# Optimization experiments

Measured on AMD Instinct MI355X. Metric: run time of the kernel, lower is better.

The kernel has to match this reference:

```python
import jax, jax.numpy as jnp
import numpy as np

B = 131072
IN_FEATS = 32
STATE = 128


def setup_inputs() -> dict:
    key = jax.random.key(0)
    k1, k2, k3, k4, k5 = jax.random.split(key, 5)
    stdv = 1.0 / np.sqrt(STATE)
    return {
        "input": jax.random.normal(k1, (B, IN_FEATS), dtype=jnp.float32),
        "old_h": jax.random.normal(k2, (B, STATE), dtype=jnp.float32),
        "old_cell": jax.random.normal(k3, (B, STATE), dtype=jnp.float32),
        "weights": jax.random.uniform(k4, (3 * STATE, IN_FEATS + STATE), dtype=jnp.float32, minval=-stdv, maxval=stdv),
        "bias": jax.random.uniform(k5, (3 * STATE,), dtype=jnp.float32, minval=-stdv, maxval=stdv),
    }


def reference(input, old_h, old_cell, weights, bias):
    # X: [B, state+in_feats] (old_h first, matching torch.cat([old_h, input], 1))
    X = jnp.concatenate([old_h, input], axis=1)
    # gate_weights: [B, 3*state] = X @ W^T + b (F.linear semantics)
    gate_weights = jnp.einsum('bf,gf->bg', X, weights) + bias
    ig_pre, og_pre, cc_pre = jnp.split(gate_weights, 3, axis=1)
    input_gate = jax.nn.sigmoid(ig_pre)
    output_gate = jax.nn.sigmoid(og_pre)
    candidate_cell = jax.nn.elu(cc_pre)
    new_cell = old_cell + candidate_cell * input_gate
    new_h = jnp.tanh(new_cell) * output_gate
    return (new_h, new_cell)
```

## Files before the change

kernel.cpp:

```cpp
#include <hip/hip_runtime.h>

#define TOTAL_B   131072
#define IN_FEATS  32
#define STATE     128
#define KDIM      160
#define BROWS     64
#define THREADS   512
#define LDSROW    384
#define GRID      512
#define ITERS     ((TOTAL_B / BROWS) / GRID)

typedef __bf16 bf16x8 __attribute__((ext_vector_type(8)));
typedef float  f32x4  __attribute__((ext_vector_type(4)));

__device__ __forceinline__ float fsigmoid(float x) { return 1.0f / (1.0f + __expf(-x)); }
__device__ __forceinline__ float ftanh(float x)    { return 2.0f / (1.0f + __expf(-2.0f * x)) - 1.0f; }

struct Xregs {
    f32x4 hlo[2], hhi[2];
    f32x4 xlo, xhi;
};

__device__ __forceinline__ void issue_x(const float* __restrict__ old_h,
                                        const float* __restrict__ xin,
                                        long b0, int t, Xregs& r)
{
    #pragma unroll
    for (int i = 0; i < 2; ++i) {
        int c   = t + i * THREADS;
        int row = c >> 4;
        int kc  = (c & 15) * 8;
        const float* p = old_h + (b0 + row) * (long)STATE + kc;
        r.hlo[i] = *(const f32x4*)p;
        r.hhi[i] = *((const f32x4*)p + 1);
    }
    if (t < 256) {
        int row = t >> 2;
        int kc  = (t & 3) * 8;
        const float* p = xin + (b0 + row) * (long)IN_FEATS + kc;
        r.xlo = *(const f32x4*)p;
        r.xhi = *((const f32x4*)p + 1);
    }
}

__device__ __forceinline__ void write_x(char* smem, int t, const Xregs& r)
{
    #pragma unroll
    for (int i = 0; i < 2; ++i) {
        int c   = t + i * THREADS;
        int row = c >> 4;
        int kc  = (c & 15) * 8;
        bf16x8 v;
        #pragma unroll
        for (int j = 0; j < 4; ++j) { v[j] = (__bf16)r.hlo[i][j]; v[j + 4] = (__bf16)r.hhi[i][j]; }
        int off = row * LDSROW + kc * 2;
        off ^= (row & 7) << 4;
        *(bf16x8*)(smem + off) = v;
    }
    if (t < 256) {
        int row = t >> 2;
        int kc  = (t & 3) * 8;
        bf16x8 v;
        #pragma unroll
        for (int j = 0; j < 4; ++j) { v[j] = (__bf16)r.xlo[j]; v[j + 4] = (__bf16)r.xhi[j]; }
        int off = row * LDSROW + (STATE + kc) * 2;
        off ^= (row & 7) << 4;
        *(bf16x8*)(smem + off) = v;
    }
}

__global__ __launch_bounds__(THREADS, 2) void lltm_fused(
    const float* __restrict__ xin,
    const float* __restrict__ old_h,
    const float* __restrict__ old_cell,
    const float* __restrict__ Wt,
    const float* __restrict__ bias,
    float* __restrict__ out)
{
    __shared__ __align__(128) char smem[BROWS * LDSROW];

    const int t    = threadIdx.x;
    const int lane = t & 63;
    const int wv   = t >> 6;
    const int l15  = lane & 15;
    const int lg   = lane >> 4;
    const int sbase = 16 * wv + 4 * lg;

    bf16x8 afrag[3][5];
    {
        const int g_lo = 16 * wv + l15;
        #pragma unroll
        for (int gt = 0; gt < 3; ++gt) {
            #pragma unroll
            for (int ks = 0; ks < 5; ++ks) {
                const float* p = Wt + (size_t)(gt * STATE + g_lo) * KDIM + ks * 32 + lg * 8;
                f32x4 lo = *(const f32x4*)p;
                f32x4 hi = *(const f32x4*)(p + 4);
                bf16x8 a;
                #pragma unroll
                for (int i = 0; i < 4; ++i) { a[i] = (__bf16)lo[i]; a[i + 4] = (__bf16)hi[i]; }
                afrag[gt][ks] = a;
            }
        }
    }
    const f32x4 b_ig = *(const f32x4*)(bias + sbase);
    const f32x4 b_og = *(const f32x4*)(bias + STATE + sbase);
    const f32x4 b_cc = *(const f32x4*)(bias + 2 * STATE + sbase);

    Xregs xr[2];
    issue_x(old_h, xin, (long)blockIdx.x * BROWS, t, xr[0]);

    #pragma unroll
    for (int it = 0; it < ITERS; ++it) {
        const long b0 = ((long)blockIdx.x + (long)it * GRID) * BROWS;

        f32x4 oc[4];
        #pragma unroll
        for (int sub = 0; sub < 4; ++sub)
            oc[sub] = *(const f32x4*)(old_cell + (b0 + sub * 16 + l15) * (long)STATE + sbase);

        write_x(smem, t, xr[it & 1]);

        if (it + 1 < ITERS)
            issue_x(old_h, xin, ((long)blockIdx.x + (long)(it + 1) * GRID) * BROWS, t, xr[(it + 1) & 1]);

        __syncthreads();

        #pragma unroll
        for (int sub = 0; sub < 4; ++sub) {
            const int brow = sub * 16 + l15;
            f32x4 acc_ig = {0.f, 0.f, 0.f, 0.f};
            f32x4 acc_og = {0.f, 0.f, 0.f, 0.f};
            f32x4 acc_cc = {0.f, 0.f, 0.f, 0.f};
            #pragma unroll
            for (int ks = 0; ks < 5; ++ks) {
                int off = brow * LDSROW + (ks * 32 + lg * 8) * 2;
                off ^= (brow & 7) << 4;
                bf16x8 bfr = *(const bf16x8*)(smem + off);
                acc_ig = __builtin_amdgcn_mfma_f32_16x16x32_bf16(afrag[0][ks], bfr, acc_ig, 0, 0, 0);
                acc_og = __builtin_amdgcn_mfma_f32_16x16x32_bf16(afrag[1][ks], bfr, acc_og, 0, 0, 0);
                acc_cc = __builtin_amdgcn_mfma_f32_16x16x32_bf16(afrag[2][ks], bfr, acc_cc, 0, 0, 0);
            }
            const long bg = b0 + sub * 16 + l15;
            f32x4 nh, nc;
            #pragma unroll
            for (int j = 0; j < 4; ++j) {
                float ig = fsigmoid(acc_ig[j] + b_ig[j]);
                float og = fsigmoid(acc_og[j] + b_og[j]);
                float cp = acc_cc[j] + b_cc[j];
                float cc = cp > 0.f ? cp : (__expf(cp) - 1.0f);
                float c2 = oc[sub][j] + cc * ig;
                nc[j] = c2;
                nh[j] = ftanh(c2) * og;
            }
            __builtin_nontemporal_store(nh, (f32x4*)(out + bg * STATE + sbase));
            __builtin_nontemporal_store(nc, (f32x4*)(out + (long)TOTAL_B * STATE + bg * STATE + sbase));
        }
        __syncthreads();
    }
}

extern "C" void kernel_launch(void* const* d_in, const int* in_sizes, int n_in,
                              void* d_out, int out_size, void* d_ws, size_t ws_size,
                              hipStream_t stream)
{
    const float* xin      = (const float*)d_in[0];
    const float* old_h    = (const float*)d_in[1];
    const float* old_cell = (const float*)d_in[2];
    const float* Wt       = (const float*)d_in[3];
    const float* bias     = (const float*)d_in[4];
    float* out = (float*)d_out;
    lltm_fused<<<GRID, THREADS, 0, stream>>>(xin, old_h, old_cell, Wt, bias, out);
}
```

Baseline: 74.20 us.

## Double-buffer LDS tile, prefetch old_cell, drop trailing barrier, raise occupancy hint

Splits the LDS staging buffer into two halves so iteration it+1 can be written while it is read, which allows the trailing __syncthreads at the end of each iteration to be removed. old_cell loads for the next tile are now issued one iteration early, alongside the old_h/input prefetch. The barrier becomes a hand-written lgkmcnt wait plus s_barrier, so it no longer waits on outstanding global loads. The launch_bounds occupancy hint goes from 2 to 4 blocks, which pressures registers (the extra oc buffer also needs more) and doubles LDS per block. That could cause spills or limit residency.

```diff
diff --git a/kernel.cpp b/kernel.cpp
--- a/kernel.cpp
+++ b/kernel.cpp
@@ -69,7 +69,7 @@
     }
 }
 
-__global__ __launch_bounds__(THREADS, 2) void lltm_fused(
+__global__ __launch_bounds__(THREADS, 4) void lltm_fused(
     const float* __restrict__ xin,
     const float* __restrict__ old_h,
     const float* __restrict__ old_cell,
@@ -77,7 +77,7 @@
     const float* __restrict__ bias,
     float* __restrict__ out)
 {
-    __shared__ __align__(128) char smem[BROWS * LDSROW];
+    __shared__ __align__(128) char smem[2][BROWS * LDSROW];
 
     const int t    = threadIdx.x;
     const int lane = t & 63;
@@ -108,24 +108,33 @@
     const f32x4 b_cc = *(const f32x4*)(bias + 2 * STATE + sbase);
 
     Xregs xr[2];
-    issue_x(old_h, xin, (long)blockIdx.x * BROWS, t, xr[0]);
+    f32x4 oc[2][4];
+    {
+        const long b0 = (long)blockIdx.x * BROWS;
+        issue_x(old_h, xin, b0, t, xr[0]);
+        #pragma unroll
+        for (int sub = 0; sub < 4; ++sub)
+            oc[0][sub] = *(const f32x4*)(old_cell + (b0 + sub * 16 + l15) * (long)STATE + sbase);
+    }
 
     #pragma unroll
     for (int it = 0; it < ITERS; ++it) {
         const long b0 = ((long)blockIdx.x + (long)it * GRID) * BROWS;
 
-        f32x4 oc[4];
-        #pragma unroll
-        for (int sub = 0; sub < 4; ++sub)
-            oc[sub] = *(const f32x4*)(old_cell + (b0 + sub * 16 + l15) * (long)STATE + sbase);
+        write_x(smem[it & 1], t, xr[it & 1]);
 
-        write_x(smem, t, xr[it & 1]);
+        if (it + 1 < ITERS) {
+            const long b1 = ((long)blockIdx.x + (long)(it + 1) * GRID) * BROWS;
+            issue_x(old_h, xin, b1, t, xr[(it + 1) & 1]);
+            #pragma unroll
+            for (int sub = 0; sub < 4; ++sub)
+                oc[(it + 1) & 1][sub] =
+                    *(const f32x4*)(old_cell + (b1 + sub * 16 + l15) * (long)STATE + sbase);
+        }
 
-        if (it + 1 < ITERS)
-            issue_x(old_h, xin, ((long)blockIdx.x + (long)(it + 1) * GRID) * BROWS, t, xr[(it + 1) & 1]);
+        asm volatile("s_waitcnt lgkmcnt(0)\n\ts_barrier" ::: "memory");
 
-        __syncthreads();
-
+        const char* sbuf = smem[it & 1];
         #pragma unroll
         for (int sub = 0; sub < 4; ++sub) {
             const int brow = sub * 16 + l15;
@@ -136,7 +145,7 @@
             for (int ks = 0; ks < 5; ++ks) {
                 int off = brow * LDSROW + (ks * 32 + lg * 8) * 2;
                 off ^= (brow & 7) << 4;
-                bf16x8 bfr = *(const bf16x8*)(smem + off);
+                bf16x8 bfr = *(const bf16x8*)(sbuf + off);
                 acc_ig = __builtin_amdgcn_mfma_f32_16x16x32_bf16(afrag[0][ks], bfr, acc_ig, 0, 0, 0);
                 acc_og = __builtin_amdgcn_mfma_f32_16x16x32_bf16(afrag[1][ks], bfr, acc_og, 0, 0, 0);
                 acc_cc = __builtin_amdgcn_mfma_f32_16x16x32_bf16(afrag[2][ks], bfr, acc_cc, 0, 0, 0);
@@ -149,14 +158,13 @@
                 float og = fsigmoid(acc_og[j] + b_og[j]);
                 float cp = acc_cc[j] + b_cc[j];
                 float cc = cp > 0.f ? cp : (__expf(cp) - 1.0f);
-                float c2 = oc[sub][j] + cc * ig;
+                float c2 = oc[it & 1][sub][j] + cc * ig;
                 nc[j] = c2;
                 nh[j] = ftanh(c2) * og;
             }
             __builtin_nontemporal_store(nh, (f32x4*)(out + bg * STATE + sbase));
             __builtin_nontemporal_store(nc, (f32x4*)(out + (long)TOTAL_B * STATE + bg * STATE + sbase));
         }
-        __syncthreads();
     }
 }
 
```

Measured after the change: 171.8 us. 2.32x slower.
